# Performance work log

Measured on AMD Instinct MI355X. Metric: run time of the kernel, lower is better.

## Reference

```python
import jax, jax.numpy as jnp
import numpy as np

RANK = 8
NUM_MORPH = 10000   # morpheme vocab (num_embeddings)
CORE_DIM = 8        # ceil(512 ** (1/3))
ORDER = 3
NUM_SURF = 50000    # word vocab (num_surfaces)
EMB_DIM = 512
LN_EPS = 1e-5
BATCH, SEQ = 8, 2048


def setup_inputs() -> dict:
    key = jax.random.key(0)
    kx, kc, kw = jax.random.split(key, 3)
    # token ids over the word vocabulary
    x = jax.random.randint(kx, (BATCH, SEQ), 0, NUM_SURF, dtype=jnp.int64)
    # word -> morpheme-id mapping, one id per tensor-train order position
    co_matrix = jax.random.randint(kc, (NUM_SURF, ORDER), 0, NUM_MORPH, dtype=jnp.int64)
    # xavier_uniform over (rank, num_morph, core_dim): fan_in = num_morph*core_dim, fan_out = rank*core_dim
    bound = float(np.sqrt(6.0 / (NUM_MORPH * CORE_DIM + RANK * CORE_DIM)))
    weight = jax.random.uniform(kw, (RANK, NUM_MORPH, CORE_DIM), dtype=jnp.float32,
                                minval=-bound, maxval=bound)
    weight = weight.at[:, 0].set(0.0)  # reset_parameters zeroes morpheme index 0
    ln_scale = jnp.ones((EMB_DIM,), dtype=jnp.float32)
    ln_bias = jnp.zeros((EMB_DIM,), dtype=jnp.float32)
    return {"x": x, "co_matrix": co_matrix, "weight": weight,
            "ln_scale": ln_scale, "ln_bias": ln_bias}


def _emb_matrix(weight, co_matrix, ln_scale, ln_bias):
    # gather all order cores at once: [rank, num_surf, order, core_dim]
    cores = weight[:, co_matrix, :]
    w = cores[:, :, 0, :]                                  # [R, S, C]
    for i in range(1, ORDER):
        # order-wise broadcast outer product, flattened feature dim grows C^i
        w = (w[:, :, :, None] * cores[:, :, i, None, :]).reshape(RANK, NUM_SURF, -1)
    w = w.sum(axis=0)[:, :EMB_DIM]                         # [S, EMB_DIM]
    mu = jnp.mean(w, axis=-1, keepdims=True)
    var = jnp.var(w, axis=-1, keepdims=True)
    return (w - mu) * jax.lax.rsqrt(var + LN_EPS) * ln_scale + ln_bias


def reference(x, co_matrix, weight, ln_scale, ln_bias):
    emb = _emb_matrix(weight, co_matrix, ln_scale, ln_bias)  # full-vocab table
    return emb[x]                                            # [B, S, EMB_DIM]
```

## Files before the change

### kernel.cpp

```cpp
#include <hip/hip_runtime.h>


#define RANK      8
#define NUM_MORPH 10000
#define EMB       512
#define LN_EPS    1e-5f
#define WPB       4
#define RSTRIDE   80000

typedef float f32x4 __attribute__((ext_vector_type(4)));

template <int CTRL>
__device__ __forceinline__ float dpp_add(float v) {
    return v + __int_as_float(__builtin_amdgcn_update_dpp(
        __float_as_int(v), __float_as_int(v), CTRL, 0xf, 0xf, false));
}
__device__ __forceinline__ float rdlane(float v, int l) {
    return __int_as_float(__builtin_amdgcn_readlane(__float_as_int(v), l));
}

__global__ __launch_bounds__(256) void morph_emb_kernel(
    const int* __restrict__ x,
    const int* __restrict__ co,
    const float* __restrict__ W,
    const float* __restrict__ lns,
    const float* __restrict__ lnb,
    float* __restrict__ out,
    int n_tok) {
    const int lane = threadIdx.x & 63;
    const int wid  = blockIdx.x * WPB + (threadIdx.x >> 6);
    const int tok  = (wid < n_tok) ? wid : (n_tok - 1);

    const int s  = __builtin_amdgcn_readfirstlane(x[tok]);
    const int m0 = __builtin_amdgcn_readfirstlane(co[s * 3 + 0]);
    const int m1 = __builtin_amdgcn_readfirstlane(co[s * 3 + 1]);
    const int m2 = __builtin_amdgcn_readfirstlane(co[s * 3 + 2]);

    const float* __restrict__ Wa = W + (size_t)m0 * 8;
    const float* __restrict__ Wb = W + (size_t)m1 * 8;
    const float* __restrict__ Wc = W + (size_t)m2 * 8;

    const int ia = lane >> 3;
    const int ib = lane & 7;

    float p[RANK];
#pragma unroll
    for (int r = 0; r < RANK; ++r)
        p[r] = Wa[r * RSTRIDE + ia] * Wb[r * RSTRIDE + ib];

    float acc[8] = {0.f, 0.f, 0.f, 0.f, 0.f, 0.f, 0.f, 0.f};
#pragma unroll
    for (int r = 0; r < RANK; ++r) {
#pragma unroll
        for (int j = 0; j < 8; ++j)
            acc[j] = fmaf(p[r], Wc[r * RSTRIDE + j], acc[j]);
    }

    float sm = 0.f, sq = 0.f;
#pragma unroll
    for (int j = 0; j < 8; ++j) { sm += acc[j]; sq += acc[j] * acc[j]; }
    sm = dpp_add<0xB1>(sm);  sq = dpp_add<0xB1>(sq);
    sm = dpp_add<0x4E>(sm);  sq = dpp_add<0x4E>(sq);
    sm = dpp_add<0x141>(sm); sq = dpp_add<0x141>(sq);
    sm = dpp_add<0x140>(sm); sq = dpp_add<0x140>(sq);
    const float tot_s = (rdlane(sm, 0) + rdlane(sm, 16)) +
                        (rdlane(sm, 32) + rdlane(sm, 48));
    const float tot_q = (rdlane(sq, 0) + rdlane(sq, 16)) +
                        (rdlane(sq, 32) + rdlane(sq, 48));
    const float mu = tot_s * (1.0f / EMB);
    const float rs = rsqrtf(tot_q * (1.0f / EMB) - mu * mu + LN_EPS);

    const int e = lane << 3;
    const f32x4 g0 = *reinterpret_cast<const f32x4*>(lns + e);
    const f32x4 g1 = *reinterpret_cast<const f32x4*>(lns + e + 4);
    const f32x4 b0 = *reinterpret_cast<const f32x4*>(lnb + e);
    const f32x4 b1 = *reinterpret_cast<const f32x4*>(lnb + e + 4);

    if (wid < n_tok) {
        f32x4 o0, o1;
        o0[0] = (acc[0] - mu) * rs * g0[0] + b0[0];
        o0[1] = (acc[1] - mu) * rs * g0[1] + b0[1];
        o0[2] = (acc[2] - mu) * rs * g0[2] + b0[2];
        o0[3] = (acc[3] - mu) * rs * g0[3] + b0[3];
        o1[0] = (acc[4] - mu) * rs * g1[0] + b1[0];
        o1[1] = (acc[5] - mu) * rs * g1[1] + b1[1];
        o1[2] = (acc[6] - mu) * rs * g1[2] + b1[2];
        o1[3] = (acc[7] - mu) * rs * g1[3] + b1[3];
        f32x4* op = reinterpret_cast<f32x4*>(out + (size_t)wid * EMB + e);
        __builtin_nontemporal_store(o0, op);
        __builtin_nontemporal_store(o1, op + 1);
    }
}

extern "C" void kernel_launch(void* const* d_in, const int* in_sizes, int n_in,
                              void* d_out, int out_size, void* d_ws, size_t ws_size,
                              hipStream_t stream) {
    const int*   x   = (const int*)d_in[0];
    const int*   co  = (const int*)d_in[1];
    const float* W   = (const float*)d_in[2];
    const float* lns = (const float*)d_in[3];
    const float* lnb = (const float*)d_in[4];
    float*       out = (float*)d_out;

    const int n_tok  = in_sizes[0];
    const int blocks = (n_tok + WPB - 1) / WPB;
    morph_emb_kernel<<<blocks, WPB * 64, 0, stream>>>(x, co, W, lns, lnb, out, n_tok);
}
```

Before: 14.39 us.

## Process two tokens per wave and broadcast third core via readlane

```diff
diff --git a/kernel.cpp b/kernel.cpp
--- a/kernel.cpp
+++ b/kernel.cpp
@@ -19,7 +19,7 @@
     return __int_as_float(__builtin_amdgcn_readlane(__float_as_int(v), l));
 }
 
-__global__ __launch_bounds__(256) void morph_emb_kernel(
+__global__ __launch_bounds__(256, 8) void morph_emb_kernel(
     const int* __restrict__ x,
     const int* __restrict__ co,
     const float* __restrict__ W,
@@ -29,46 +29,34 @@
     int n_tok) {
     const int lane = threadIdx.x & 63;
     const int wid  = blockIdx.x * WPB + (threadIdx.x >> 6);
-    const int tok  = (wid < n_tok) ? wid : (n_tok - 1);
+    const int t0   = wid * 2;
+    const int tA   = (t0     < n_tok) ? t0     : (n_tok - 1);
+    const int tB   = (t0 + 1 < n_tok) ? t0 + 1 : (n_tok - 1);
 
-    const int s  = __builtin_amdgcn_readfirstlane(x[tok]);
-    const int m0 = __builtin_amdgcn_readfirstlane(co[s * 3 + 0]);
-    const int m1 = __builtin_amdgcn_readfirstlane(co[s * 3 + 1]);
-    const int m2 = __builtin_amdgcn_readfirstlane(co[s * 3 + 2]);
-
-    const float* __restrict__ Wa = W + (size_t)m0 * 8;
-    const float* __restrict__ Wb = W + (size_t)m1 * 8;
-    const float* __restrict__ Wc = W + (size_t)m2 * 8;
+    const int sA  = x[tA];
+    const int sB  = x[tB];
+    const int mA0 = co[sA * 3 + 0], mA1 = co[sA * 3 + 1], mA2 = co[sA * 3 + 2];
+    const int mB0 = co[sB * 3 + 0], mB1 = co[sB * 3 + 1], mB2 = co[sB * 3 + 2];
 
     const int ia = lane >> 3;
     const int ib = lane & 7;
 
-    float p[RANK];
-#pragma unroll
-    for (int r = 0; r < RANK; ++r)
-        p[r] = Wa[r * RSTRIDE + ia] * Wb[r * RSTRIDE + ib];
+    const float cA =
+        W[(size_t)ia * RSTRIDE + (size_t)mA2 * 8 + ib];
+    const float cB =
+        W[(size_t)ia * RSTRIDE + (size_t)mB2 * 8 + ib];
 
-    float acc[8] = {0.f, 0.f, 0.f, 0.f, 0.f, 0.f, 0.f, 0.f};
+    const float* paA = W + (size_t)mA0 * 8 + ia;
+    const float* pbA = W + (size_t)mA1 * 8 + ib;
+    const float* paB = W + (size_t)mB0 * 8 + ia;
+    const float* pbB = W + (size_t)mB1 * 8 + ib;
+
+    float pA[RANK], pB[RANK];
 #pragma unroll
     for (int r = 0; r < RANK; ++r) {
-#pragma unroll
-        for (int j = 0; j < 8; ++j)
-            acc[j] = fmaf(p[r], Wc[r * RSTRIDE + j], acc[j]);
+        pA[r] = paA[r * RSTRIDE] * pbA[r * RSTRIDE];
+        pB[r] = paB[r * RSTRIDE] * pbB[r * RSTRIDE];
     }
-
-    float sm = 0.f, sq = 0.f;
-#pragma unroll
-    for (int j = 0; j < 8; ++j) { sm += acc[j]; sq += acc[j] * acc[j]; }
-    sm = dpp_add<0xB1>(sm);  sq = dpp_add<0xB1>(sq);
-    sm = dpp_add<0x4E>(sm);  sq = dpp_add<0x4E>(sq);
-    sm = dpp_add<0x141>(sm); sq = dpp_add<0x141>(sq);
-    sm = dpp_add<0x140>(sm); sq = dpp_add<0x140>(sq);
-    const float tot_s = (rdlane(sm, 0) + rdlane(sm, 16)) +
-                        (rdlane(sm, 32) + rdlane(sm, 48));
-    const float tot_q = (rdlane(sq, 0) + rdlane(sq, 16)) +
-                        (rdlane(sq, 32) + rdlane(sq, 48));
-    const float mu = tot_s * (1.0f / EMB);
-    const float rs = rsqrtf(tot_q * (1.0f / EMB) - mu * mu + LN_EPS);
 
     const int e = lane << 3;
     const f32x4 g0 = *reinterpret_cast<const f32x4*>(lns + e);
@@ -76,19 +64,78 @@
     const f32x4 b0 = *reinterpret_cast<const f32x4*>(lnb + e);
     const f32x4 b1 = *reinterpret_cast<const f32x4*>(lnb + e + 4);
 
-    if (wid < n_tok) {
-        f32x4 o0, o1;
-        o0[0] = (acc[0] - mu) * rs * g0[0] + b0[0];
-        o0[1] = (acc[1] - mu) * rs * g0[1] + b0[1];
-        o0[2] = (acc[2] - mu) * rs * g0[2] + b0[2];
-        o0[3] = (acc[3] - mu) * rs * g0[3] + b0[3];
-        o1[0] = (acc[4] - mu) * rs * g1[0] + b1[0];
-        o1[1] = (acc[5] - mu) * rs * g1[1] + b1[1];
-        o1[2] = (acc[6] - mu) * rs * g1[2] + b1[2];
-        o1[3] = (acc[7] - mu) * rs * g1[3] + b1[3];
-        f32x4* op = reinterpret_cast<f32x4*>(out + (size_t)wid * EMB + e);
-        __builtin_nontemporal_store(o0, op);
-        __builtin_nontemporal_store(o1, op + 1);
+    float accA[8] = {0.f, 0.f, 0.f, 0.f, 0.f, 0.f, 0.f, 0.f};
+#pragma unroll
+    for (int r = 0; r < RANK; ++r) {
+#pragma unroll
+        for (int j = 0; j < 8; ++j)
+            accA[j] = fmaf(pA[r], rdlane(cA, r * 8 + j), accA[j]);
+    }
+    float smA = 0.f, sqA = 0.f;
+#pragma unroll
+    for (int j = 0; j < 8; ++j) { smA += accA[j]; sqA += accA[j] * accA[j]; }
+    smA = dpp_add<0xB1>(smA);  sqA = dpp_add<0xB1>(sqA);
+    smA = dpp_add<0x4E>(smA);  sqA = dpp_add<0x4E>(sqA);
+    smA = dpp_add<0x141>(smA); sqA = dpp_add<0x141>(sqA);
+    smA = dpp_add<0x140>(smA); sqA = dpp_add<0x140>(sqA);
+    {
+        const float ts = (rdlane(smA, 0) + rdlane(smA, 16)) +
+                         (rdlane(smA, 32) + rdlane(smA, 48));
+        const float tq = (rdlane(sqA, 0) + rdlane(sqA, 16)) +
+                         (rdlane(sqA, 32) + rdlane(sqA, 48));
+        const float mu = ts * (1.0f / EMB);
+        const float rs = rsqrtf(tq * (1.0f / EMB) - mu * mu + LN_EPS);
+        if (t0 < n_tok) {
+            f32x4 o0, o1;
+            o0[0] = (accA[0] - mu) * rs * g0[0] + b0[0];
+            o0[1] = (accA[1] - mu) * rs * g0[1] + b0[1];
+            o0[2] = (accA[2] - mu) * rs * g0[2] + b0[2];
+            o0[3] = (accA[3] - mu) * rs * g0[3] + b0[3];
+            o1[0] = (accA[4] - mu) * rs * g1[0] + b1[0];
+            o1[1] = (accA[5] - mu) * rs * g1[1] + b1[1];
+            o1[2] = (accA[6] - mu) * rs * g1[2] + b1[2];
+            o1[3] = (accA[7] - mu) * rs * g1[3] + b1[3];
+            f32x4* op = reinterpret_cast<f32x4*>(out + (size_t)t0 * EMB + e);
+            __builtin_nontemporal_store(o0, op);
+            __builtin_nontemporal_store(o1, op + 1);
+        }
+    }
+
+    float accB[8] = {0.f, 0.f, 0.f, 0.f, 0.f, 0.f, 0.f, 0.f};
+#pragma unroll
+    for (int r = 0; r < RANK; ++r) {
+#pragma unroll
+        for (int j = 0; j < 8; ++j)
+            accB[j] = fmaf(pB[r], rdlane(cB, r * 8 + j), accB[j]);
+    }
+    float smB = 0.f, sqB = 0.f;
+#pragma unroll
+    for (int j = 0; j < 8; ++j) { smB += accB[j]; sqB += accB[j] * accB[j]; }
+    smB = dpp_add<0xB1>(smB);  sqB = dpp_add<0xB1>(sqB);
+    smB = dpp_add<0x4E>(smB);  sqB = dpp_add<0x4E>(sqB);
+    smB = dpp_add<0x141>(smB); sqB = dpp_add<0x141>(sqB);
+    smB = dpp_add<0x140>(smB); sqB = dpp_add<0x140>(sqB);
+    {
+        const float ts = (rdlane(smB, 0) + rdlane(smB, 16)) +
+                         (rdlane(smB, 32) + rdlane(smB, 48));
+        const float tq = (rdlane(sqB, 0) + rdlane(sqB, 16)) +
+                         (rdlane(sqB, 32) + rdlane(sqB, 48));
+        const float mu = ts * (1.0f / EMB);
+        const float rs = rsqrtf(tq * (1.0f / EMB) - mu * mu + LN_EPS);
+        if (t0 + 1 < n_tok) {
+            f32x4 o0, o1;
+            o0[0] = (accB[0] - mu) * rs * g0[0] + b0[0];
+            o0[1] = (accB[1] - mu) * rs * g0[1] + b0[1];
+            o0[2] = (accB[2] - mu) * rs * g0[2] + b0[2];
+            o0[3] = (accB[3] - mu) * rs * g0[3] + b0[3];
+            o1[0] = (accB[4] - mu) * rs * g1[0] + b1[0];
+            o1[1] = (accB[5] - mu) * rs * g1[1] + b1[1];
+            o1[2] = (accB[6] - mu) * rs * g1[2] + b1[2];
+            o1[3] = (accB[7] - mu) * rs * g1[3] + b1[3];
+            f32x4* op = reinterpret_cast<f32x4*>(out + (size_t)(t0 + 1) * EMB + e);
+            __builtin_nontemporal_store(o0, op);
+            __builtin_nontemporal_store(o1, op + 1);
+        }
     }
 }
 
@@ -103,6 +150,6 @@
     float*       out = (float*)d_out;
 
     const int n_tok  = in_sizes[0];
-    const int blocks = (n_tok + WPB - 1) / WPB;
+    const int blocks = (n_tok / 2 + WPB - 1) / WPB;
     morph_emb_kernel<<<blocks, WPB * 64, 0, stream>>>(x, co, W, lns, lnb, out, n_tok);
 }
```

Measured after the change: 16.23 us. 12.8% more time.
